# Performance work log

Measured on AMD Instinct MI355X. Metric: run time of the kernel, lower is better.

Reference implementation:

```python
import jax, jax.numpy as jnp
import numpy as np

N, E = 25000, 400000
NF, EF, HNF, HEF = 32, 32, 128, 128
NOUT, EOUT = 32, 32
D_N, D_E = HNF + NF, HEF + EF  # concat dims fed to the GNN layer


def _glorot(key, shape):
    return jax.random.normal(key, shape, jnp.float32) / np.sqrt(shape[0])


def setup_inputs() -> dict:
    key = jax.random.key(0)
    ks = jax.random.split(key, 10)
    return {
        "nf": jax.random.normal(ks[0], (N, NF), jnp.float32),
        "ef": jax.random.normal(ks[1], (E, EF), jnp.float32),
        "src": jax.random.randint(ks[2], (E,), 0, N),
        "dst": jax.random.randint(ks[3], (E,), 0, N),
        # AttnMPNNLayer params: edge model, attention logit model, node model
        "W_edge": _glorot(ks[4], (2 * D_N + D_E, HEF)),
        "b_edge": jnp.zeros((HEF,), jnp.float32),
        "W_attn": _glorot(ks[5], (2 * D_N + D_E, 1)),
        "b_attn": jnp.zeros((1,), jnp.float32),
        "W_node": _glorot(ks[6], (D_N + HEF, HNF)),
        "b_node": jnp.zeros((HNF,), jnp.float32),
        # output heads (MLP with num_neurons=[] -> single Linear)
        "W_nout": _glorot(ks[7], (HNF, NOUT)),
        "b_nout": jnp.zeros((NOUT,), jnp.float32),
        "W_eout": _glorot(ks[8], (HEF, EOUT)),
        "b_eout": jnp.zeros((EOUT,), jnp.float32),
        "n_iters": 3,
    }


def _attn_mpnn_layer(hnf, hef, src, dst, W_edge, b_edge, W_attn, b_attn, W_node, b_node):
    """Attention message passing: gather endpoints, edge MLP + attn logit,
    edge-softmax over incoming edges (per dst node), scatter-aggregate, node MLP."""
    n = hnf.shape[0]
    e_in = jnp.concatenate([hnf[src], hnf[dst], hef], axis=-1)   # [E, 2*D_N + D_E]
    m = jax.nn.relu(e_in @ W_edge + b_edge)                      # [E, HEF] new edge feats
    logit = (e_in @ W_attn + b_attn)[:, 0]                       # [E]
    # numerically stable edge softmax grouped by destination node
    lmax = jax.ops.segment_max(logit, dst, num_segments=n)
    lmax = jnp.where(jnp.isfinite(lmax), lmax, 0.0)              # isolated nodes -> 0
    a = jnp.exp(logit - lmax[dst])
    denom = jax.ops.segment_sum(a, dst, num_segments=n)
    alpha = a / jnp.maximum(denom[dst], 1e-16)
    agg = jax.ops.segment_sum(alpha[:, None] * m, dst, num_segments=n)  # [N, HEF]
    un = jax.nn.relu(jnp.concatenate([hnf, agg], axis=-1) @ W_node + b_node)  # [N, HNF]
    return un, m


def reference(nf, ef, src, dst, W_edge, b_edge, W_attn, b_attn, W_node, b_node,
              W_nout, b_nout, W_eout, b_eout, n_iters):
    hnf = jnp.zeros((nf.shape[0], HNF), nf.dtype)
    hef = jnp.zeros((ef.shape[0], HEF), ef.dtype)
    for _ in range(n_iters):
        hnf = jnp.concatenate([hnf, nf], axis=-1)   # input re-injection
        hef = jnp.concatenate([hef, ef], axis=-1)
        hnf, hef = _attn_mpnn_layer(hnf, hef, src, dst,
                                    W_edge, b_edge, W_attn, b_attn, W_node, b_node)
    unf = hnf @ W_nout + b_nout
    uef = hef @ W_eout + b_eout
    return unf, uef
```

## Files before the change

kernel.cpp:

```cpp
#include <hip/hip_runtime.h>


#define GN 25000
#define GE 400000
#define NODE_BLKS 196
#define EDGE_BLKS 6250
#define HEAD_EBLKS 3125

typedef unsigned short u16;
typedef __attribute__((ext_vector_type(8))) short bf16x8;
typedef __attribute__((ext_vector_type(4))) float f32x4;

__device__ inline float b2f(u16 v) {
  union { unsigned int u; float f; } x; x.u = ((unsigned int)v) << 16; return x.f;
}
__device__ inline u16 f2b(float f) {
  union { float f; unsigned int u; } x; x.f = f;
  unsigned int u = x.u;
  u += 0x7fffu + ((u >> 16) & 1u);
  return (u16)(u >> 16);
}

__global__ void detect_dtype(const void* nf, int* flag) {
  if (blockIdx.x == 0 && threadIdx.x == 0) {
    const u16* p = (const u16*)nf;
    int cnt = 0;
    for (int i = 0; i < 512; i += 2) {
      int e = (p[i] >> 7) & 0xFF;
      if (e >= 0x70 && e <= 0x85) cnt++;
    }
    *flag = (cnt < 128) ? 1 : 0;
  }
}

__global__ void convert_kernel(const void* src, u16* dst, long n, const int* flag) {
  int f32 = *flag;
  long i = (long)blockIdx.x * blockDim.x + threadIdx.x;
  long stride = (long)gridDim.x * blockDim.x;
  for (; i < n; i += stride)
    dst[i] = f32 ? f2b(((const float*)src)[i]) : ((const u16*)src)[i];
}

__global__ void gather_ef(const void* ef, const int* eid, u16* efc, const int* flag) {
  int f32 = *flag;
  long idx = (long)blockIdx.x * blockDim.x + threadIdx.x;
  long ntot = (long)GE * 4;
  if (idx >= ntot) return;
  long j = idx >> 2;
  int g = (int)(idx & 3) * 8;
  long e = eid[j];
  uint4 out;
  if (f32) {
    const float* pf = (const float*)ef + e * 32 + g;
    float4 a = ((const float4*)pf)[0];
    float4 b = ((const float4*)pf)[1];
    unsigned int* ov = (unsigned int*)&out;
    ov[0] = (unsigned int)f2b(a.x) | ((unsigned int)f2b(a.y) << 16);
    ov[1] = (unsigned int)f2b(a.z) | ((unsigned int)f2b(a.w) << 16);
    ov[2] = (unsigned int)f2b(b.x) | ((unsigned int)f2b(b.y) << 16);
    ov[3] = (unsigned int)f2b(b.z) | ((unsigned int)f2b(b.w) << 16);
  } else {
    out = *(const uint4*)((const u16*)ef + e * 32 + g);
  }
  *(uint4*)(efc + j * 32 + g) = out;
}

__global__ void prep_weights(const void* We, const void* Wn, const void* Wa,
                             const void* Won, const void* Woe,
                             const void* be, const void* ba, const void* bn,
                             const void* bno, const void* beo,
                             u16* WeT, u16* WnpT, u16* WnuT, u16* WoN, u16* WoE,
                             u16* Wac, u16* bec, u16* bac, u16* bnc, u16* bnoc, u16* beoc,
                             const int* flag) {
  int f32 = *flag;
  auto ld = [&](const void* p, long i) -> u16 {
    return f32 ? f2b(((const float*)p)[i]) : ((const u16*)p)[i];
  };
  int tid = blockIdx.x * blockDim.x + threadIdx.x;
  int nt = gridDim.x * blockDim.x;
  for (int i = tid; i < 128 * 160; i += nt) { int n = i / 160, k = i % 160; WeT[i] = ld(We, (long)(320 + k) * 128 + n); }
  for (int i = tid; i < 256 * 160; i += nt) {
    int c = i / 160, k = i % 160;
    WnpT[i] = (c < 128) ? ld(We, (long)k * 128 + c) : ld(We, (long)(160 + k) * 128 + (c - 128));
  }
  for (int i = tid; i < 128 * 288; i += nt) { int c = i / 288, k = i % 288; WnuT[i] = ld(Wn, (long)k * 128 + c); }
  for (int i = tid; i < 32 * 128; i += nt) {
    int c = i / 128, k = i % 128;
    WoN[i] = ld(Won, (long)k * 32 + c);
    WoE[i] = ld(Woe, (long)k * 32 + c);
  }
  for (int i = tid; i < 480; i += nt) Wac[i] = ld(Wa, i);
  for (int i = tid; i < 128; i += nt) { bec[i] = ld(be, i); bnc[i] = ld(bn, i); }
  for (int i = tid; i < 32; i += nt) { bnoc[i] = ld(bno, i); beoc[i] = ld(beo, i); }
  if (tid == 0) bac[0] = ld(ba, 0);
}

__global__ void hist_kernel(const int* dst, int* counts, int n) {
  for (int e = blockIdx.x * blockDim.x + threadIdx.x; e < n; e += gridDim.x * blockDim.x)
    atomicAdd(&counts[dst[e]], 1);
}

__global__ __launch_bounds__(1024) void scan_kernel(int* cursor, int* rowptr, int n) {
  __shared__ int part[1024];
  int t = threadIdx.x;
  int per = (n + 1023) / 1024;
  int lo = t * per;
  int hi = lo + per; if (hi > n) hi = n;
  if (lo > n) lo = n;
  int s = 0;
  for (int i = lo; i < hi; ++i) s += cursor[i];
  part[t] = s;
  __syncthreads();
  for (int off = 1; off < 1024; off <<= 1) {
    int v = (t >= off) ? part[t - off] : 0;
    __syncthreads();
    part[t] += v;
    __syncthreads();
  }
  int run = (t > 0) ? part[t - 1] : 0;
  for (int i = lo; i < hi; ++i) {
    int c = cursor[i];
    cursor[i] = run;
    rowptr[i + 1] = run + c;
    run += c;
  }
  if (t == 0) rowptr[0] = 0;
}

__global__ void fill_kernel(const int* src, const int* dst, int* cursor, int* eid,
                            int* srcs, int* dsts, int n) {
  for (int e = blockIdx.x * blockDim.x + threadIdx.x; e < n; e += gridDim.x * blockDim.x) {
    int d = dst[e];
    int p = atomicAdd(&cursor[d], 1);
    eid[p] = e;
    srcs[p] = src[e];
    dsts[p] = d;
  }
}

__global__ __launch_bounds__(256)
void node_proj(const u16* HNF, const u16* nf, const u16* WnpT, const u16* W_attn,
               u16* Xs, u16* Xd, float* as_, float* ad_, int kc0, int nrows) {
  __shared__ union {
    struct { __align__(16) u16 A[128][40]; __align__(16) u16 B[128][40]; } st;
    u16 C[128][130];
  } sm;
  __shared__ float dotbuf[128][2];
  int sel = blockIdx.y, blk = blockIdx.x, tid = threadIdx.x;
  int lane = tid & 63, wv = tid >> 6, wr = wv & 1, wc = wv >> 1;
  const u16* BT = WnpT + sel * 128 * 160;
  u16* OUT = sel ? Xd : Xs;
  float* AOUT = sel ? ad_ : as_;
  const u16* wa = W_attn + sel * 160;
  f32x4 acc[4][4];
  f32x4 zf = {0.f, 0.f, 0.f, 0.f};
  for (int i = 0; i < 4; ++i) for (int j = 0; j < 4; ++j) acc[i][j] = zf;
  float dp = 0.f;
  int arow = tid >> 1, ahalf = (tid & 1) * 16;
  int r0 = blk * 128;
  for (int kc = kc0; kc < 5; ++kc) {
    {
      int r = r0 + arow;
      uint4 v0 = make_uint4(0, 0, 0, 0), v1 = make_uint4(0, 0, 0, 0);
      if (r < nrows) {
        const uint4* p = (kc < 4) ? (const uint4*)(HNF + (size_t)r * 128 + kc * 32 + ahalf)
                                  : (const uint4*)(nf + (size_t)r * 32 + ahalf);
        v0 = p[0]; v1 = p[1];
      }
      *(uint4*)&sm.st.A[arow][ahalf] = v0;
      *(uint4*)&sm.st.A[arow][ahalf + 8] = v1;
    }
    {
      const uint4* p = (const uint4*)(BT + arow * 160 + kc * 32 + ahalf);
      uint4 v0 = p[0], v1 = p[1];
      *(uint4*)&sm.st.B[arow][ahalf] = v0;
      *(uint4*)&sm.st.B[arow][ahalf + 8] = v1;
    }
    __syncthreads();
    {
      float s = 0.f;
      for (int j = 0; j < 16; ++j) s += b2f(sm.st.A[arow][ahalf + j]) * b2f(wa[kc * 32 + ahalf + j]);
      dp += s;
    }
    int q = lane >> 4, l16 = lane & 15;
    bf16x8 af[4], bfr[4];
    for (int i = 0; i < 4; ++i) af[i] = *(const bf16x8*)&sm.st.A[wr * 64 + i * 16 + l16][q * 8];
    for (int j = 0; j < 4; ++j) bfr[j] = *(const bf16x8*)&sm.st.B[wc * 64 + j * 16 + l16][q * 8];
    for (int i = 0; i < 4; ++i)
      for (int j = 0; j < 4; ++j)
        acc[i][j] = __builtin_amdgcn_mfma_f32_16x16x32_bf16(af[i], bfr[j], acc[i][j], 0, 0, 0);
    __syncthreads();
  }
  dotbuf[arow][tid & 1] = dp;
  {
    int q = lane >> 4, l16 = lane & 15;
    for (int i = 0; i < 4; ++i)
      for (int j = 0; j < 4; ++j) {
        int col = wc * 64 + j * 16 + l16;
        for (int rr = 0; rr < 4; ++rr) {
          int row = wr * 64 + i * 16 + q * 4 + rr;
          sm.C[row][col] = f2b(acc[i][j][rr]);
        }
      }
  }
  __syncthreads();
  if (tid < 128) {
    int r = r0 + tid;
    if (r < nrows) AOUT[r] = dotbuf[tid][0] + dotbuf[tid][1];
  }
  {
    int r = tid >> 1, h = (tid & 1) * 64;
    int rg = r0 + r;
    if (rg < nrows) {
      uint4* po = (uint4*)(OUT + (size_t)rg * 128 + h);
      for (int k = 0; k < 8; ++k) {
        unsigned int a0 = *(const unsigned int*)&sm.C[r][h + k * 8];
        unsigned int a1 = *(const unsigned int*)&sm.C[r][h + k * 8 + 2];
        unsigned int a2 = *(const unsigned int*)&sm.C[r][h + k * 8 + 4];
        unsigned int a3 = *(const unsigned int*)&sm.C[r][h + k * 8 + 6];
        po[k] = make_uint4(a0, a1, a2, a3);
      }
    }
  }
}

template <int KC0>
__global__ __launch_bounds__(256, 4)
void edge_fused(u16* HEF, const u16* ef, const u16* WeT, const u16* W_attn,
                const u16* b_edge, const u16* b_attn, const int* srcs, const int* dsts,
                const u16* Xs, const u16* Xd, const float* as_, const float* ad_,
                float* logit) {
  __shared__ float C[64][65];
  __shared__ float dotbuf[64];
  int blk = blockIdx.x, tid = threadIdx.x;
  int lane = tid & 63, wv = tid >> 6, wr = wv & 1, wc = wv >> 1;
  int q = lane >> 4, l16 = lane & 15;
  f32x4 acc[2][4];
  f32x4 zf = {0.f, 0.f, 0.f, 0.f};
  for (int i = 0; i < 2; ++i) for (int j = 0; j < 4; ++j) acc[i][j] = zf;
  float dp[2] = {0.f, 0.f};
  long e0 = (long)blk * 64;
  const u16* wa = W_attn + 320;
  long ar = e0 + wr * 32 + l16;
  const u16* aH0 = HEF + ar * 128 + q * 8;
  const u16* aH1 = aH0 + 16 * 128;
  const u16* aE0 = ef + ar * 32 + q * 8;
  const u16* aE1 = aE0 + 16 * 32;
  const u16* bW = WeT + (size_t)(wc * 64 + l16) * 160 + q * 8;

  bf16x8 afp[2][2], bfp[2][4];
#pragma unroll
  for (int j = 0; j < 4; ++j)
    bfp[KC0 & 1][j] = *(const bf16x8*)(bW + (size_t)j * 16 * 160 + KC0 * 32);
  afp[KC0 & 1][0] = (KC0 < 4) ? *(const bf16x8*)(aH0 + KC0 * 32) : *(const bf16x8*)aE0;
  afp[KC0 & 1][1] = (KC0 < 4) ? *(const bf16x8*)(aH1 + KC0 * 32) : *(const bf16x8*)aE1;

#pragma unroll
  for (int kc = KC0; kc < 5; ++kc) {
    int cur = kc & 1, nxt = cur ^ 1;
    if (kc < 4) {
      int kn = kc + 1;
      afp[nxt][0] = (kn < 4) ? *(const bf16x8*)(aH0 + kn * 32) : *(const bf16x8*)aE0;
      afp[nxt][1] = (kn < 4) ? *(const bf16x8*)(aH1 + kn * 32) : *(const bf16x8*)aE1;
#pragma unroll
      for (int j = 0; j < 4; ++j)
        bfp[nxt][j] = *(const bf16x8*)(bW + (size_t)j * 16 * 160 + kn * 32);
    }
    if (wc == 0) {
      bf16x8 wv8 = *(const bf16x8*)&wa[kc * 32 + q * 8];
      float wf[8];
      for (int j = 0; j < 8; ++j) wf[j] = b2f((u16)wv8[j]);
      for (int i = 0; i < 2; ++i)
        for (int j = 0; j < 8; ++j) dp[i] += b2f((u16)afp[cur][i][j]) * wf[j];
    }
    for (int i = 0; i < 2; ++i)
      for (int j = 0; j < 4; ++j)
        acc[i][j] = __builtin_amdgcn_mfma_f32_16x16x32_bf16(afp[cur][i], bfp[cur][j], acc[i][j], 0, 0, 0);
  }
  if (wc == 0) {
    for (int i = 0; i < 2; ++i) {
      dp[i] += __shfl_xor(dp[i], 16);
      dp[i] += __shfl_xor(dp[i], 32);
    }
    if (q == 0)
      for (int i = 0; i < 2; ++i) dotbuf[wr * 32 + i * 16 + l16] = dp[i];
  }
  int r = tid >> 2, qh = tid & 3;
  long e = e0 + r;
  int s = srcs[e], d = dsts[e];
#pragma unroll
  for (int p = 0; p < 2; ++p) {
    int cb = p * 64 + qh * 16;
    const uint4* ps = (const uint4*)(Xs + (size_t)s * 128 + cb);
    const uint4* pd = (const uint4*)(Xd + (size_t)d * 128 + cb);
    uint4 gs0 = ps[0], gs1 = ps[1], gd0 = pd[0], gd1 = pd[1];
    __syncthreads();
    if (wc == p) {
      for (int i = 0; i < 2; ++i)
        for (int j = 0; j < 4; ++j) {
          int col = j * 16 + l16;
          float bb = b2f(b_edge[p * 64 + col]);
          for (int rr = 0; rr < 4; ++rr)
            C[wr * 32 + i * 16 + q * 4 + rr][col] = acc[i][j][rr] + bb;
        }
    }
    __syncthreads();
    if (p == 0 && tid < 64) {
      long ee = e0 + tid;
      logit[ee] = dotbuf[tid] + as_[srcs[ee]] + ad_[dsts[ee]] + b2f(b_attn[0]);
    }
    unsigned int us[8], ud[8];
    *(uint4*)&us[0] = gs0; *(uint4*)&us[4] = gs1;
    *(uint4*)&ud[0] = gd0; *(uint4*)&ud[4] = gd1;
    unsigned int ov[8];
    for (int w = 0; w < 8; ++w) {
      float c0 = C[r][qh * 16 + 2 * w];
      float c1 = C[r][qh * 16 + 2 * w + 1];
      float v0 = c0 + b2f((u16)(us[w] & 0xffffu)) + b2f((u16)(ud[w] & 0xffffu));
      float v1 = c1 + b2f((u16)(us[w] >> 16)) + b2f((u16)(ud[w] >> 16));
      ov[w] = (unsigned int)f2b(fmaxf(v0, 0.f)) | ((unsigned int)f2b(fmaxf(v1, 0.f)) << 16);
    }
    uint4* po = (uint4*)(HEF + e * 128 + cb);
    po[0] = *(uint4*)&ov[0];
    po[1] = *(uint4*)&ov[4];
  }
}

__global__ __launch_bounds__(256)
void aggregate(const int* rowptr, const float* logit, const u16* M, u16* AGG, int nrows) {
  int gw = (blockIdx.x * blockDim.x + threadIdx.x) >> 6;
  int lane = threadIdx.x & 63;
  if (gw >= nrows) return;
  int beg = rowptr[gw], end = rowptr[gw + 1];
  int sub = lane >> 3, cl = lane & 7;
  float mx = -1e30f;
  for (int j = beg + lane; j < end; j += 64) mx = fmaxf(mx, logit[j]);
  for (int off = 32; off > 0; off >>= 1) mx = fmaxf(mx, __shfl_xor(mx, off));
  float acc[16];
  for (int t = 0; t < 16; ++t) acc[t] = 0.f;
  float denom = 0.f;
  float wc = 0.f;
  uint4 m0c = make_uint4(0, 0, 0, 0), m1c = make_uint4(0, 0, 0, 0);
  {
    int j = beg + sub;
    if (j < end) {
      wc = __expf(logit[j] - mx);
      const uint4* mp = (const uint4*)(M + (size_t)j * 128 + cl * 16);
      m0c = mp[0]; m1c = mp[1];
    }
  }
  for (int j0 = beg; j0 < end; j0 += 8) {
    float wn = 0.f;
    uint4 m0n = make_uint4(0, 0, 0, 0), m1n = make_uint4(0, 0, 0, 0);
    int jn = j0 + 8 + sub;
    if (jn < end) {
      wn = __expf(logit[jn] - mx);
      const uint4* mp = (const uint4*)(M + (size_t)jn * 128 + cl * 16);
      m0n = mp[0]; m1n = mp[1];
    }
    denom += wc;
    const unsigned int* mw0 = (const unsigned int*)&m0c;
    const unsigned int* mw1 = (const unsigned int*)&m1c;
    for (int t = 0; t < 4; ++t) {
      acc[2 * t]     += wc * b2f((u16)(mw0[t] & 0xffffu));
      acc[2 * t + 1] += wc * b2f((u16)(mw0[t] >> 16));
      acc[8 + 2 * t]     += wc * b2f((u16)(mw1[t] & 0xffffu));
      acc[8 + 2 * t + 1] += wc * b2f((u16)(mw1[t] >> 16));
    }
    wc = wn; m0c = m0n; m1c = m1n;
  }
  denom += __shfl_xor(denom, 8);
  denom += __shfl_xor(denom, 16);
  denom += __shfl_xor(denom, 32);
  for (int t = 0; t < 16; ++t) {
    acc[t] += __shfl_xor(acc[t], 8);
    acc[t] += __shfl_xor(acc[t], 16);
    acc[t] += __shfl_xor(acc[t], 32);
  }
  float inv = 1.0f / fmaxf(denom, 1e-16f);
  if (sub == 0) {
    unsigned int ov[8];
    for (int t = 0; t < 8; ++t)
      ov[t] = (unsigned int)f2b(acc[2 * t] * inv) | ((unsigned int)f2b(acc[2 * t + 1] * inv) << 16);
    uint4* po = (uint4*)(AGG + (size_t)gw * 128 + cl * 16);
    po[0] = *(uint4*)&ov[0];
    po[1] = *(uint4*)&ov[4];
  }
}

__global__ __launch_bounds__(256)
void node_update(u16* HNF, const u16* nf, const u16* AGG, const u16* WnuT,
                 const u16* b_node, int kc0, int nrows) {
  __shared__ union {
    struct { __align__(16) u16 A[128][40]; __align__(16) u16 B[128][40]; } st;
    u16 C[128][130];
  } sm;
  int blk = blockIdx.x, tid = threadIdx.x;
  int lane = tid & 63, wv = tid >> 6, wr = wv & 1, wc = wv >> 1;
  f32x4 acc[4][4];
  f32x4 zf = {0.f, 0.f, 0.f, 0.f};
  for (int i = 0; i < 4; ++i) for (int j = 0; j < 4; ++j) acc[i][j] = zf;
  int arow = tid >> 1, ahalf = (tid & 1) * 16;
  int r0 = blk * 128;
  for (int kc = kc0; kc < 9; ++kc) {
    {
      int r = r0 + arow;
      uint4 v0 = make_uint4(0, 0, 0, 0), v1 = make_uint4(0, 0, 0, 0);
      if (r < nrows) {
        const u16* p;
        if (kc < 4) p = HNF + (size_t)r * 128 + kc * 32 + ahalf;
        else if (kc == 4) p = nf + (size_t)r * 32 + ahalf;
        else p = AGG + (size_t)r * 128 + (kc - 5) * 32 + ahalf;
        v0 = ((const uint4*)p)[0];
        v1 = ((const uint4*)p)[1];
      }
      *(uint4*)&sm.st.A[arow][ahalf] = v0;
      *(uint4*)&sm.st.A[arow][ahalf + 8] = v1;
    }
    {
      const uint4* p = (const uint4*)(WnuT + arow * 288 + kc * 32 + ahalf);
      uint4 v0 = p[0], v1 = p[1];
      *(uint4*)&sm.st.B[arow][ahalf] = v0;
      *(uint4*)&sm.st.B[arow][ahalf + 8] = v1;
    }
    __syncthreads();
    int q = lane >> 4, l16 = lane & 15;
    bf16x8 af[4], bfr[4];
    for (int i = 0; i < 4; ++i) af[i] = *(const bf16x8*)&sm.st.A[wr * 64 + i * 16 + l16][q * 8];
    for (int j = 0; j < 4; ++j) bfr[j] = *(const bf16x8*)&sm.st.B[wc * 64 + j * 16 + l16][q * 8];
    for (int i = 0; i < 4; ++i)
      for (int j = 0; j < 4; ++j)
        acc[i][j] = __builtin_amdgcn_mfma_f32_16x16x32_bf16(af[i], bfr[j], acc[i][j], 0, 0, 0);
    __syncthreads();
  }
  int q = lane >> 4, l16 = lane & 15;
  for (int i = 0; i < 4; ++i)
    for (int j = 0; j < 4; ++j) {
      int col = wc * 64 + j * 16 + l16;
      float bb = b2f(b_node[col]);
      for (int rr = 0; rr < 4; ++rr) {
        int row = wr * 64 + i * 16 + q * 4 + rr;
        sm.C[row][col] = f2b(fmaxf(acc[i][j][rr] + bb, 0.f));
      }
    }
  __syncthreads();
  {
    int r = tid >> 1, h = (tid & 1) * 64;
    int rg = r0 + r;
    if (rg < nrows) {
      uint4* po = (uint4*)(HNF + (size_t)rg * 128 + h);
      for (int k = 0; k < 8; ++k) {
        unsigned int a0 = *(const unsigned int*)&sm.C[r][h + k * 8];
        unsigned int a1 = *(const unsigned int*)&sm.C[r][h + k * 8 + 2];
        unsigned int a2 = *(const unsigned int*)&sm.C[r][h + k * 8 + 4];
        unsigned int a3 = *(const unsigned int*)&sm.C[r][h + k * 8 + 6];
        po[k] = make_uint4(a0, a1, a2, a3);
      }
    }
  }
}

__global__ __launch_bounds__(256)
void head_kernel(const u16* IN, const u16* WT, const u16* bias, float* OUT, long R,
                 const int* remap) {
  __shared__ __align__(16) u16 Asm[128][40];
  __shared__ __align__(16) u16 Bsm[32][40];
  int blk = blockIdx.x, tid = threadIdx.x;
  int lane = tid & 63, wv = tid >> 6;
  f32x4 acc[2][2];
  f32x4 zf = {0.f, 0.f, 0.f, 0.f};
  for (int i = 0; i < 2; ++i) for (int j = 0; j < 2; ++j) acc[i][j] = zf;
  int arow = tid >> 1, ahalf = (tid & 1) * 16;
  long r0 = (long)blk * 128;
  for (int kc = 0; kc < 4; ++kc) {
    {
      long r = r0 + arow;
      uint4 v0 = make_uint4(0, 0, 0, 0), v1 = make_uint4(0, 0, 0, 0);
      if (r < R) {
        const uint4* p = (const uint4*)(IN + r * 128 + kc * 32 + ahalf);
        v0 = p[0]; v1 = p[1];
      }
      *(uint4*)&Asm[arow][ahalf] = v0;
      *(uint4*)&Asm[arow][ahalf + 8] = v1;
    }
    if (tid < 64) {
      const uint4* p = (const uint4*)(WT + arow * 128 + kc * 32 + ahalf);
      uint4 v0 = p[0], v1 = p[1];
      *(uint4*)&Bsm[arow][ahalf] = v0;
      *(uint4*)&Bsm[arow][ahalf + 8] = v1;
    }
    __syncthreads();
    int q = lane >> 4, l16 = lane & 15;
    bf16x8 af[2], bfr[2];
    for (int i = 0; i < 2; ++i) af[i] = *(const bf16x8*)&Asm[wv * 32 + i * 16 + l16][q * 8];
    for (int j = 0; j < 2; ++j) bfr[j] = *(const bf16x8*)&Bsm[j * 16 + l16][q * 8];
    for (int i = 0; i < 2; ++i)
      for (int j = 0; j < 2; ++j)
        acc[i][j] = __builtin_amdgcn_mfma_f32_16x16x32_bf16(af[i], bfr[j], acc[i][j], 0, 0, 0);
    __syncthreads();
  }
  int q = lane >> 4, l16 = lane & 15;
  for (int i = 0; i < 2; ++i)
    for (int rr = 0; rr < 4; ++rr) {
      long r = r0 + wv * 32 + i * 16 + q * 4 + rr;
      if (r < R) {
        long ro = remap ? (long)remap[r] : r;
        for (int j = 0; j < 2; ++j) {
          int col = j * 16 + l16;
          OUT[ro * 32 + col] = acc[i][j][rr] + b2f(bias[col]);
        }
      }
    }
}

extern "C" void kernel_launch(void* const* d_in, const int* in_sizes, int n_in,
                              void* d_out, int out_size, void* d_ws, size_t ws_size,
                              hipStream_t stream) {
  const size_t REQUIRED = 160000000;
  if (ws_size < REQUIRED) return;

  const void* nf_r = d_in[0];
  const void* ef_r = d_in[1];
  const int* src = (const int*)d_in[2];
  const int* dst = (const int*)d_in[3];

  char* ws = (char*)d_ws;
  auto alloc = [&](size_t bytes) {
    char* p = ws;
    ws += (bytes + 255) & ~(size_t)255;
    return p;
  };
  u16* HEF = (u16*)alloc((size_t)GE * 128 * 2);
  u16* HNF = (u16*)alloc((size_t)GN * 128 * 2);
  u16* Xs = (u16*)alloc((size_t)GN * 128 * 2);
  u16* Xd = (u16*)alloc((size_t)GN * 128 * 2);
  float* as_ = (float*)alloc((size_t)GN * 4);
  float* ad_ = (float*)alloc((size_t)GN * 4);
  float* logit = (float*)alloc((size_t)GE * 4);
  int* rowptr = (int*)alloc((size_t)(GN + 1) * 4);
  int* cursor = (int*)alloc((size_t)GN * 4);
  int* eid = (int*)alloc((size_t)GE * 4);
  int* srcs = (int*)alloc((size_t)GE * 4);
  int* dsts = (int*)alloc((size_t)GE * 4);
  u16* WeT = (u16*)alloc(128 * 160 * 2);
  u16* WnpT = (u16*)alloc(256 * 160 * 2);
  u16* WnuT = (u16*)alloc(128 * 288 * 2);
  u16* WoN = (u16*)alloc(32 * 128 * 2);
  u16* WoE = (u16*)alloc(32 * 128 * 2);
  u16* nfc = (u16*)alloc((size_t)GN * 32 * 2);
  u16* efc = (u16*)alloc((size_t)GE * 32 * 2);
  u16* bec = (u16*)alloc(128 * 2);
  u16* Wac = (u16*)alloc(480 * 2);
  u16* bac = (u16*)alloc(2);
  u16* bnc = (u16*)alloc(128 * 2);
  u16* bnoc = (u16*)alloc(32 * 2);
  u16* beoc = (u16*)alloc(32 * 2);
  int* dflag = (int*)alloc(4);
  u16* AGG = Xs;

  detect_dtype<<<1, 64, 0, stream>>>(nf_r, dflag);
  hipMemsetAsync(cursor, 0, (size_t)GN * 4, stream);
  hist_kernel<<<1563, 256, 0, stream>>>(dst, cursor, GE);
  scan_kernel<<<1, 1024, 0, stream>>>(cursor, rowptr, GN);
  fill_kernel<<<1563, 256, 0, stream>>>(src, dst, cursor, eid, srcs, dsts, GE);

  convert_kernel<<<784, 256, 0, stream>>>(nf_r, nfc, (long)GN * 32, dflag);
  gather_ef<<<6250, 256, 0, stream>>>(ef_r, eid, efc, dflag);
  prep_weights<<<128, 256, 0, stream>>>(d_in[4], d_in[8], d_in[6], d_in[10], d_in[12],
                                        d_in[5], d_in[7], d_in[9], d_in[11], d_in[13],
                                        WeT, WnpT, WnuT, WoN, WoE,
                                        Wac, bec, bac, bnc, bnoc, beoc, dflag);

  for (int iter = 0; iter < 3; ++iter) {
    int kc0 = (iter == 0) ? 4 : 0;
    dim3 npgrid(NODE_BLKS, 2);
    node_proj<<<npgrid, 256, 0, stream>>>(HNF, nfc, WnpT, Wac, Xs, Xd, as_, ad_, kc0, GN);
    if (iter == 0)
      edge_fused<4><<<EDGE_BLKS, 256, 0, stream>>>(HEF, efc, WeT, Wac, bec, bac, srcs, dsts,
                                                   Xs, Xd, as_, ad_, logit);
    else
      edge_fused<0><<<EDGE_BLKS, 256, 0, stream>>>(HEF, efc, WeT, Wac, bec, bac, srcs, dsts,
                                                   Xs, Xd, as_, ad_, logit);
    aggregate<<<(GN + 3) / 4, 256, 0, stream>>>(rowptr, logit, HEF, AGG, GN);
    node_update<<<NODE_BLKS, 256, 0, stream>>>(HNF, nfc, AGG, WnuT, bnc, kc0, GN);
  }

  float* out_nf = (float*)d_out;
  float* out_ef = (float*)d_out + (size_t)GN * 32;
  head_kernel<<<NODE_BLKS, 256, 0, stream>>>(HNF, WoN, bnoc, out_nf, GN, nullptr);
  head_kernel<<<HEAD_EBLKS, 256, 0, stream>>>(HEF, WoE, beoc, out_ef, GE, eid);
}
```

Before: 648.1 us.

## Register-prefetch next K tile in GEMM kernels; stage edge A tile through LDS

```diff
diff --git a/kernel.cpp b/kernel.cpp
--- a/kernel.cpp
+++ b/kernel.cpp
@@ -158,23 +158,32 @@
   float dp = 0.f;
   int arow = tid >> 1, ahalf = (tid & 1) * 16;
   int r0 = blk * 128;
+  int ra = r0 + arow;
+  uint4 va0 = make_uint4(0, 0, 0, 0), va1 = make_uint4(0, 0, 0, 0), vb0, vb1;
+  {
+    if (ra < nrows) {
+      const uint4* p = (kc0 < 4) ? (const uint4*)(HNF + (size_t)ra * 128 + kc0 * 32 + ahalf)
+                                 : (const uint4*)(nf + (size_t)ra * 32 + ahalf);
+      va0 = p[0]; va1 = p[1];
+    }
+    const uint4* pb = (const uint4*)(BT + arow * 160 + kc0 * 32 + ahalf);
+    vb0 = pb[0]; vb1 = pb[1];
+  }
   for (int kc = kc0; kc < 5; ++kc) {
-    {
-      int r = r0 + arow;
-      uint4 v0 = make_uint4(0, 0, 0, 0), v1 = make_uint4(0, 0, 0, 0);
-      if (r < nrows) {
-        const uint4* p = (kc < 4) ? (const uint4*)(HNF + (size_t)r * 128 + kc * 32 + ahalf)
-                                  : (const uint4*)(nf + (size_t)r * 32 + ahalf);
-        v0 = p[0]; v1 = p[1];
-      }
-      *(uint4*)&sm.st.A[arow][ahalf] = v0;
-      *(uint4*)&sm.st.A[arow][ahalf + 8] = v1;
-    }
-    {
-      const uint4* p = (const uint4*)(BT + arow * 160 + kc * 32 + ahalf);
-      uint4 v0 = p[0], v1 = p[1];
-      *(uint4*)&sm.st.B[arow][ahalf] = v0;
-      *(uint4*)&sm.st.B[arow][ahalf + 8] = v1;
+    *(uint4*)&sm.st.A[arow][ahalf] = va0;
+    *(uint4*)&sm.st.A[arow][ahalf + 8] = va1;
+    *(uint4*)&sm.st.B[arow][ahalf] = vb0;
+    *(uint4*)&sm.st.B[arow][ahalf + 8] = vb1;
+    if (kc < 4) {
+      int kn = kc + 1;
+      va0 = make_uint4(0, 0, 0, 0); va1 = make_uint4(0, 0, 0, 0);
+      if (ra < nrows) {
+        const uint4* p = (kn < 4) ? (const uint4*)(HNF + (size_t)ra * 128 + kn * 32 + ahalf)
+                                  : (const uint4*)(nf + (size_t)ra * 32 + ahalf);
+        va0 = p[0]; va1 = p[1];
+      }
+      const uint4* pb = (const uint4*)(BT + arow * 160 + kn * 32 + ahalf);
+      vb0 = pb[0]; vb1 = pb[1];
     }
     __syncthreads();
     {
@@ -230,7 +239,10 @@
                 const u16* b_edge, const u16* b_attn, const int* srcs, const int* dsts,
                 const u16* Xs, const u16* Xd, const float* as_, const float* ad_,
                 float* logit) {
-  __shared__ float C[64][65];
+  __shared__ union {
+    __align__(16) u16 A[2][64][40];
+    float C[64][65];
+  } sm;
   __shared__ float dotbuf[64];
   int blk = blockIdx.x, tid = threadIdx.x;
   int lane = tid & 63, wv = tid >> 6, wr = wv & 1, wc = wv >> 1;
@@ -240,42 +252,41 @@
   for (int i = 0; i < 2; ++i) for (int j = 0; j < 4; ++j) acc[i][j] = zf;
   float dp[2] = {0.f, 0.f};
   long e0 = (long)blk * 64;
+  long ea = e0 + (tid >> 2);
+  int qp = (tid & 3) * 8;
   const u16* wa = W_attn + 320;
-  long ar = e0 + wr * 32 + l16;
-  const u16* aH0 = HEF + ar * 128 + q * 8;
-  const u16* aH1 = aH0 + 16 * 128;
-  const u16* aE0 = ef + ar * 32 + q * 8;
-  const u16* aE1 = aE0 + 16 * 32;
-  const u16* bW = WeT + (size_t)(wc * 64 + l16) * 160 + q * 8;
-
-  bf16x8 afp[2][2], bfp[2][4];
+
+  uint4 va = (KC0 < 4) ? *(const uint4*)(HEF + ea * 128 + KC0 * 32 + qp)
+                       : *(const uint4*)(ef + ea * 32 + qp);
+  bf16x8 bfp[2][4];
 #pragma unroll
   for (int j = 0; j < 4; ++j)
-    bfp[KC0 & 1][j] = *(const bf16x8*)(bW + (size_t)j * 16 * 160 + KC0 * 32);
-  afp[KC0 & 1][0] = (KC0 < 4) ? *(const bf16x8*)(aH0 + KC0 * 32) : *(const bf16x8*)aE0;
-  afp[KC0 & 1][1] = (KC0 < 4) ? *(const bf16x8*)(aH1 + KC0 * 32) : *(const bf16x8*)aE1;
+    bfp[KC0 & 1][j] = *(const bf16x8*)(WeT + (size_t)(wc * 64 + j * 16 + l16) * 160 + KC0 * 32 + q * 8);
 
 #pragma unroll
   for (int kc = KC0; kc < 5; ++kc) {
-    int cur = kc & 1, nxt = cur ^ 1;
+    int buf = kc & 1;
+    *(uint4*)&sm.A[buf][tid >> 2][qp] = va;
     if (kc < 4) {
-      int kn = kc + 1;
-      afp[nxt][0] = (kn < 4) ? *(const bf16x8*)(aH0 + kn * 32) : *(const bf16x8*)aE0;
-      afp[nxt][1] = (kn < 4) ? *(const bf16x8*)(aH1 + kn * 32) : *(const bf16x8*)aE1;
+      va = (kc + 1 < 4) ? *(const uint4*)(HEF + ea * 128 + (kc + 1) * 32 + qp)
+                        : *(const uint4*)(ef + ea * 32 + qp);
 #pragma unroll
       for (int j = 0; j < 4; ++j)
-        bfp[nxt][j] = *(const bf16x8*)(bW + (size_t)j * 16 * 160 + kn * 32);
-    }
+        bfp[(kc + 1) & 1][j] = *(const bf16x8*)(WeT + (size_t)(wc * 64 + j * 16 + l16) * 160 + (kc + 1) * 32 + q * 8);
+    }
+    __syncthreads();
+    bf16x8 af[2];
+    for (int i = 0; i < 2; ++i) af[i] = *(const bf16x8*)&sm.A[buf][wr * 32 + i * 16 + l16][q * 8];
     if (wc == 0) {
       bf16x8 wv8 = *(const bf16x8*)&wa[kc * 32 + q * 8];
       float wf[8];
       for (int j = 0; j < 8; ++j) wf[j] = b2f((u16)wv8[j]);
       for (int i = 0; i < 2; ++i)
-        for (int j = 0; j < 8; ++j) dp[i] += b2f((u16)afp[cur][i][j]) * wf[j];
+        for (int j = 0; j < 8; ++j) dp[i] += b2f((u16)af[i][j]) * wf[j];
     }
     for (int i = 0; i < 2; ++i)
       for (int j = 0; j < 4; ++j)
-        acc[i][j] = __builtin_amdgcn_mfma_f32_16x16x32_bf16(afp[cur][i], bfp[cur][j], acc[i][j], 0, 0, 0);
+        acc[i][j] = __builtin_amdgcn_mfma_f32_16x16x32_bf16(af[i], bfp[buf][j], acc[i][j], 0, 0, 0);
   }
   if (wc == 0) {
     for (int i = 0; i < 2; ++i) {
@@ -301,7 +312,7 @@
           int col = j * 16 + l16;
           float bb = b2f(b_edge[p * 64 + col]);
           for (int rr = 0; rr < 4; ++rr)
-            C[wr * 32 + i * 16 + q * 4 + rr][col] = acc[i][j][rr] + bb;
+            sm.C[wr * 32 + i * 16 + q * 4 + rr][col] = acc[i][j][rr] + bb;
         }
     }
     __syncthreads();
@@ -314,8 +325,8 @@
     *(uint4*)&ud[0] = gd0; *(uint4*)&ud[4] = gd1;
     unsigned int ov[8];
     for (int w = 0; w < 8; ++w) {
-      float c0 = C[r][qh * 16 + 2 * w];
-      float c1 = C[r][qh * 16 + 2 * w + 1];
+      float c0 = sm.C[r][qh * 16 + 2 * w];
+      float c1 = sm.C[r][qh * 16 + 2 * w + 1];
       float v0 = c0 + b2f((u16)(us[w] & 0xffffu)) + b2f((u16)(ud[w] & 0xffffu));
       float v1 = c1 + b2f((u16)(us[w] >> 16)) + b2f((u16)(ud[w] >> 16));
       ov[w] = (unsigned int)f2b(fmaxf(v0, 0.f)) | ((unsigned int)f2b(fmaxf(v1, 0.f)) << 16);
@@ -402,26 +413,35 @@
   for (int i = 0; i < 4; ++i) for (int j = 0; j < 4; ++j) acc[i][j] = zf;
   int arow = tid >> 1, ahalf = (tid & 1) * 16;
   int r0 = blk * 128;
+  int ra = r0 + arow;
+  auto asrc = [&](int kc) -> const u16* {
+    if (kc < 4) return HNF + (size_t)ra * 128 + kc * 32 + ahalf;
+    if (kc == 4) return nf + (size_t)ra * 32 + ahalf;
+    return AGG + (size_t)ra * 128 + (kc - 5) * 32 + ahalf;
+  };
+  uint4 va0 = make_uint4(0, 0, 0, 0), va1 = make_uint4(0, 0, 0, 0), vb0, vb1;
+  {
+    if (ra < nrows) {
+      const uint4* p = (const uint4*)asrc(kc0);
+      va0 = p[0]; va1 = p[1];
+    }
+    const uint4* pb = (const uint4*)(WnuT + arow * 288 + kc0 * 32 + ahalf);
+    vb0 = pb[0]; vb1 = pb[1];
+  }
   for (int kc = kc0; kc < 9; ++kc) {
-    {
-      int r = r0 + arow;
-      uint4 v0 = make_uint4(0, 0, 0, 0), v1 = make_uint4(0, 0, 0, 0);
-      if (r < nrows) {
-        const u16* p;
-        if (kc < 4) p = HNF + (size_t)r * 128 + kc * 32 + ahalf;
-        else if (kc == 4) p = nf + (size_t)r * 32 + ahalf;
-        else p = AGG + (size_t)r * 128 + (kc - 5) * 32 + ahalf;
-        v0 = ((const uint4*)p)[0];
-        v1 = ((const uint4*)p)[1];
-      }
-      *(uint4*)&sm.st.A[arow][ahalf] = v0;
-      *(uint4*)&sm.st.A[arow][ahalf + 8] = v1;
-    }
-    {
-      const uint4* p = (const uint4*)(WnuT + arow * 288 + kc * 32 + ahalf);
-      uint4 v0 = p[0], v1 = p[1];
-      *(uint4*)&sm.st.B[arow][ahalf] = v0;
-      *(uint4*)&sm.st.B[arow][ahalf + 8] = v1;
+    *(uint4*)&sm.st.A[arow][ahalf] = va0;
+    *(uint4*)&sm.st.A[arow][ahalf + 8] = va1;
+    *(uint4*)&sm.st.B[arow][ahalf] = vb0;
+    *(uint4*)&sm.st.B[arow][ahalf + 8] = vb1;
+    if (kc < 8) {
+      int kn = kc + 1;
+      va0 = make_uint4(0, 0, 0, 0); va1 = make_uint4(0, 0, 0, 0);
+      if (ra < nrows) {
+        const uint4* p = (const uint4*)asrc(kn);
+        va0 = p[0]; va1 = p[1];
+      }
+      const uint4* pb = (const uint4*)(WnuT + arow * 288 + kn * 32 + ahalf);
+      vb0 = pb[0]; vb1 = pb[1];
     }
     __syncthreads();
     int q = lane >> 4, l16 = lane & 15;
@@ -472,22 +492,37 @@
   for (int i = 0; i < 2; ++i) for (int j = 0; j < 2; ++j) acc[i][j] = zf;
   int arow = tid >> 1, ahalf = (tid & 1) * 16;
   long r0 = (long)blk * 128;
+  long ra = r0 + arow;
+  uint4 va0 = make_uint4(0, 0, 0, 0), va1 = make_uint4(0, 0, 0, 0);
+  uint4 vb0 = make_uint4(0, 0, 0, 0), vb1 = make_uint4(0, 0, 0, 0);
+  {
+    if (ra < R) {
+      const uint4* p = (const uint4*)(IN + ra * 128 + 0 * 32 + ahalf);
+      va0 = p[0]; va1 = p[1];
+    }
+    if (tid < 64) {
+      const uint4* p = (const uint4*)(WT + arow * 128 + 0 * 32 + ahalf);
+      vb0 = p[0]; vb1 = p[1];
+    }
+  }
   for (int kc = 0; kc < 4; ++kc) {
-    {
-      long r = r0 + arow;
-      uint4 v0 = make_uint4(0, 0, 0, 0), v1 = make_uint4(0, 0, 0, 0);
-      if (r < R) {
-        const uint4* p = (const uint4*)(IN + r * 128 + kc * 32 + ahalf);
-        v0 = p[0]; v1 = p[1];
-      }
-      *(uint4*)&Asm[arow][ahalf] = v0;
-      *(uint4*)&Asm[arow][ahalf + 8] = v1;
-    }
+    *(uint4*)&Asm[arow][ahalf] = va0;
+    *(uint4*)&Asm[arow][ahalf + 8] = va1;
     if (tid < 64) {
-      const uint4* p = (const uint4*)(WT + arow * 128 + kc * 32 + ahalf);
-      uint4 v0 = p[0], v1 = p[1];
-      *(uint4*)&Bsm[arow][ahalf] = v0;
-      *(uint4*)&Bsm[arow][ahalf + 8] = v1;
+      *(uint4*)&Bsm[arow][ahalf] = vb0;
+      *(uint4*)&Bsm[arow][ahalf + 8] = vb1;
+    }
+    if (kc < 3) {
+      int kn = kc + 1;
+      va0 = make_uint4(0, 0, 0, 0); va1 = make_uint4(0, 0, 0, 0);
+      if (ra < R) {
+        const uint4* p = (const uint4*)(IN + ra * 128 + kn * 32 + ahalf);
+        va0 = p[0]; va1 = p[1];
+      }
+      if (tid < 64) {
+        const uint4* p = (const uint4*)(WT + arow * 128 + kn * 32 + ahalf);
+        vb0 = p[0]; vb1 = p[1];
+      }
     }
     __syncthreads();
     int q = lane >> 4, l16 = lane & 15;
```

Measured after the change: 603.6 us. 6.9% less time.
